# Performance work log

Hardware: AMD Instinct MI355X
Metric: run time of the kernel (lower is better)

The kernel has to match this reference:

```python
import jax, jax.numpy as jnp
import numpy as np

N_PIX = 4_194_304      # native emulator wavelength grid length
N_BINS = 350_000       # number of data wavelength bins (searchsorted labels)
MEDIAN_WL = 10500.0    # Angstroms, np.median(wl_bin_edges)
C_KMS = 299792.458     # speed of light, km/s
PI_SRC = 3.1415926654  # the (slightly off) pi literal used in the source
KERNEL_TAPS = 901      # torch.arange(-4.5, 4.51, 0.01)


def _conv_same(flux, kernel):
    """conv1d with padding='same'; kernels are symmetric so corr == conv."""
    half = kernel.shape[0] // 2
    out = jax.lax.conv_general_dilated(
        flux[None, None, :], kernel[None, None, :],
        window_strides=(1,), padding=[(half, half)])
    return out[0, 0]


def setup_inputs() -> dict:
    key = jax.random.key(0)
    k1, k2 = jax.random.split(key)
    return {
        "high_res_model": jax.random.uniform(k1, (N_PIX,), dtype=jnp.float32),
        "ln_sigma_angs": jnp.asarray(-2.3, dtype=jnp.float32),
        "ln_vsini": jnp.asarray(2.89, dtype=jnp.float32),
        "segment_ids": jnp.sort(jax.random.randint(k2, (N_PIX,), 0, N_BINS)),
    }


def reference(high_res_model, ln_sigma_angs, ln_vsini, segment_ids):
    dt = high_res_model.dtype
    grid = jnp.linspace(-4.5, 4.5, KERNEL_TAPS).astype(dt)
    sigma_angs = 0.01 + jnp.exp(ln_sigma_angs)
    vsini = 0.9 + jnp.exp(ln_vsini)

    # --- rotational broadening kernel ---
    x = (C_KMS * grid / MEDIAN_WL) / vsini
    x2 = jnp.minimum(x * x, 1.0)                     # torch.clamp(x2, max=1)
    inside = x2 < 0.99999999
    safe_x2 = jnp.where(inside, x2, 0.0)             # avoid sqrt(neg)/nan-grad
    rot_kernel = jnp.where(inside, 2.0 * jnp.sqrt(1.0 - safe_x2), 0.0)
    rot_kernel = rot_kernel / jnp.sum(rot_kernel)
    rot = _conv_same(high_res_model, rot_kernel)

    # --- instrumental (Gaussian) broadening kernel ---
    gauss = (1.0 / (sigma_angs * jnp.sqrt(jnp.asarray(2.0 * PI_SRC, dt)))
             * jnp.exp(-0.5 * grid * grid / (sigma_angs * sigma_angs)) * 0.01)
    conv = _conv_same(rot, gauss)

    # --- resample to data: fused segment mean (replaces split+per-bin mean) ---
    sums = jax.ops.segment_sum(conv, segment_ids, num_segments=N_BINS)
    counts = jax.ops.segment_sum(jnp.ones_like(conv), segment_ids,
                                 num_segments=N_BINS)
    means = sums / jnp.maximum(counts, 1.0)
    return jnp.clip(means, 0.0, 1.0)[1:-1]
```

## Files before the change

### kernel.cpp

```cpp
#include <hip/hip_runtime.h>
#include <hip/hip_bf16.h>

#define TAPS 901
#define CB 256
#define R 11
#define NGRP 22
#define NK (R * NGRP)
#define OPB (CB * R)
#define STAGE_N 3060
#define TILE 3072
#define WPAD 12

__device__ __forceinline__ float4 ld4(const float* p) {
  return *reinterpret_cast<const float4*>(p);
}

__global__ __launch_bounds__(1024) void prep(
    const float* __restrict__ lns, const float* __restrict__ lnv,
    const float* __restrict__ flux, const int* __restrict__ ids,
    float* __restrict__ comb_w, int* __restrict__ bounds,
    float* __restrict__ sums, int n) {
  __shared__ float rk[1024], gk[1024], red[1024];
  __shared__ float ck[2048];
  __shared__ int sb[8];
  const int t = threadIdx.x;
  if (t < 8) sb[t] = (t & 1) ? -1 : 4096;
  __syncthreads();

  const float sigma = 0.01f + expf(lns[0]);
  const float vsini = 0.9f + expf(lnv[0]);

  float rv = 0.f, gv = 0.f;
  if (t < TAPS) {
    float g = -4.5f + 0.01f * (float)t;
    float x = (299792.458f * g / 10500.0f) / vsini;
    float x2 = fminf(x * x, 1.0f);
    if (x2 < 1.0f) rv = 2.0f * sqrtf(1.0f - x2);
    gv = (1.0f / (sigma * sqrtf(2.0f * 3.1415926654f))) *
         expf(-0.5f * g * g / (sigma * sigma)) * 0.01f;
  }
  red[t] = rv;
  __syncthreads();
  for (int s = 512; s > 0; s >>= 1) {
    if (t < s) red[t] += red[t + s];
    __syncthreads();
  }
  const float rsum = red[0];

  const float rw = (t < TAPS) ? rv / rsum : 0.f;
  rk[t] = rw;
  gk[t] = gv;
  if (t < TAPS) {
    if (rw != 0.f)          { atomicMin(&sb[0], t); atomicMax(&sb[1], t); }
    if (fabsf(gv) > 1e-10f) { atomicMin(&sb[2], t); atomicMax(&sb[3], t); }
  }
  __syncthreads();
  const int rlo = sb[0], rhi = sb[1], glo = sb[2], ghi = sb[3];
  int flo = 450 - glo; if (flo < 0) flo = 0;
  int fhi = ghi - 450; if (fhi < 0) fhi = 0;

  if (blockIdx.x == 0) {
    for (int t2 = t; t2 < 2048; t2 += 1024) {
      float c = 0.f;
      if (t2 <= 1800) {
        int jmin = rlo > t2 - ghi ? rlo : t2 - ghi;
        int jmax = rhi < t2 - glo ? rhi : t2 - glo;
        for (int j = jmin; j <= jmax; ++j) c += rk[j] * gk[t2 - j];
      }
      ck[t2] = c;
      comb_w[t2] = c;
      if (t2 <= 1800 && fabsf(c) > 1e-12f) { atomicMin(&sb[4], t2); atomicMax(&sb[5], t2); }
    }
    __syncthreads();
    if (t == 0) {
      int clo = sb[4], chi = sb[5];
      if (chi < clo) { clo = 900; chi = 900; }
      while (chi - (clo & ~3) + 1 > NK) {
        if (fabsf(ck[clo]) <= fabsf(ck[chi])) ++clo; else --chi;
      }
      bounds[0] = clo & ~3; bounds[1] = flo; bounds[2] = fhi;
    }
  } else if (blockIdx.x == 1) {
    const int m = flo + fhi;
    float* rbuf = ck;
    for (int j = t; j < m; j += 1024) {
      float s = 0.f;
      int j0 = 450 - j > rlo ? 450 - j : rlo;
      for (int j2 = j0; j2 <= rhi; ++j2) s += rk[j2] * flux[j + j2 - 450];
      rbuf[j] = s;
    }
    __syncthreads();
    for (int i = t; i < flo; i += 1024) {
      float c = 0.f;
      int k0 = 450 - i > glo ? 450 - i : glo;
      for (int k = k0; k <= ghi; ++k) c += gk[k] * rbuf[i + k - 450];
      atomicAdd(&sums[ids[i]], c);
    }
  } else {
    const int m = flo + fhi;
    float* rbuf = ck;
    const int jbase = n - m;
    for (int jj = t; jj < m; jj += 1024) {
      int j = jbase + jj;
      float s = 0.f;
      int j2hi = n - 1 + 450 - j < rhi ? n - 1 + 450 - j : rhi;
      for (int j2 = rlo; j2 <= j2hi; ++j2) s += rk[j2] * flux[j + j2 - 450];
      rbuf[jj] = s;
    }
    __syncthreads();
    for (int ii = t; ii < fhi; ii += 1024) {
      int i = n - fhi + ii;
      float c = 0.f;
      int khi = n - 1 + 450 - i < ghi ? n - 1 + 450 - i : ghi;
      for (int k = glo; k <= khi; ++k) c += gk[k] * rbuf[i + k - 450 - jbase];
      atomicAdd(&sums[ids[i]], c);
    }
  }
}

__global__ __launch_bounds__(CB) void conv_scatter(
    const float* __restrict__ flux, const float* __restrict__ comb_w,
    const int* __restrict__ bounds, const int* __restrict__ ids,
    float* __restrict__ sums, int* __restrict__ bstart, int n, int nbins) {
  __shared__ __align__(16) float lds[TILE];
  __shared__ __align__(16) float wl[NGRP * WPAD];
  const int tid = threadIdx.x;
  const int clo4 = __builtin_amdgcn_readfirstlane(bounds[0]);
  const int flo  = __builtin_amdgcn_readfirstlane(bounds[1]);
  const int fhi  = __builtin_amdgcn_readfirstlane(bounds[2]);
  const int blockBase = blockIdx.x * OPB;
  const int start = blockBase - 900 + clo4;

  if (start >= 0 && start + STAGE_N <= n) {
    for (int j = tid * 4; j < STAGE_N; j += CB * 4)
      *reinterpret_cast<float4*>(&lds[j]) = ld4(flux + start + j);
  } else {
    for (int j = tid * 4; j < STAGE_N; j += CB * 4) {
      int g = start + j;
      float4 v;
      v.x = (unsigned)g       < (unsigned)n ? flux[g]     : 0.f;
      v.y = (unsigned)(g + 1) < (unsigned)n ? flux[g + 1] : 0.f;
      v.z = (unsigned)(g + 2) < (unsigned)n ? flux[g + 2] : 0.f;
      v.w = (unsigned)(g + 3) < (unsigned)n ? flux[g + 3] : 0.f;
      *reinterpret_cast<float4*>(&lds[j]) = v;
    }
  }
  for (int k = tid; k < NGRP * WPAD; k += CB) {
    const int g = k / WPAD, u = k % WPAD;
    wl[k] = (u < R) ? comb_w[clo4 + g * R + u] : 0.f;
  }
  __syncthreads();

  const int idx0 = tid * R;
  float win[R];
#pragma unroll
  for (int r = 0; r < R; ++r) win[r] = lds[idx0 + r];
  float acc[R];
#pragma unroll
  for (int r = 0; r < R; ++r) acc[r] = 0.f;

  const float4* wl4 = reinterpret_cast<const float4*>(wl);
#define TAP(u, wv)                                                     \
  {                                                                    \
    _Pragma("unroll") for (int r = 0; r < R; ++r)                      \
        acc[r] = fmaf(wv, win[((u) + r) % R], acc[r]);                 \
    win[u] = lds[idx0 + kk + (u) + R];                                 \
  }
  float4 n0 = wl4[0], n1 = wl4[1], n2 = wl4[2];
#pragma unroll 2
  for (int g = 0; g < NGRP; ++g) {
    const int kk = g * R;
    const float4 q0 = n0, q1 = n1, q2 = n2;
    if (g + 1 < NGRP) {
      n0 = wl4[(g + 1) * 3 + 0];
      n1 = wl4[(g + 1) * 3 + 1];
      n2 = wl4[(g + 1) * 3 + 2];
    }
    TAP(0, q0.x)  TAP(1, q0.y)  TAP(2, q0.z)  TAP(3, q0.w)
    TAP(4, q1.x)  TAP(5, q1.y)  TAP(6, q1.z)  TAP(7, q1.w)
    TAP(8, q2.x)  TAP(9, q2.y)  TAP(10, q2.z)
  }
#undef TAP

  const int base = blockBase + idx0;
  const int loskip = flo - base;
  const int hicap = (n - fhi) - base;
  int prev = (base > 0) ? ((base < n) ? ids[base - 1] : 0) : -1;
  int cur = -1; float run = 0.f;
#pragma unroll
  for (int r = 0; r < R; ++r) {
    const int p = base + r;
    if (p < n) {
      const int id = ids[p];
      if (id != prev) {
        for (int b = prev + 1; b <= id; ++b) bstart[b] = p;
        prev = id;
      }
      if (r >= loskip && r < hicap) {
        if (id == cur) {
          run += acc[r];
        } else {
          if (cur >= 0) atomicAdd(&sums[cur], run);
          cur = id; run = acc[r];
        }
      }
    }
  }
  if (cur >= 0) atomicAdd(&sums[cur], run);
  if (base < n && base + R > n - 1) {
    for (int b = prev + 1; b < nbins; ++b) bstart[b] = n;
  }
}

__global__ __launch_bounds__(256) void seg_mean(
    const float* __restrict__ sums, const int* __restrict__ bstart,
    float* __restrict__ out, int out_n) {
  const int gid = blockIdx.x * blockDim.x + threadIdx.x;
  if (gid >= out_n) return;
  const int b = gid + 1;
  const int c = bstart[b + 1] - bstart[b];
  const float mean = sums[b] / (float)(c > 1 ? c : 1);
  out[gid] = fminf(fmaxf(mean, 0.f), 1.f);
}

extern "C" void kernel_launch(void* const* d_in, const int* in_sizes, int n_in,
                              void* d_out, int out_size, void* d_ws,
                              size_t ws_size, hipStream_t stream) {
  const float* flux = (const float*)d_in[0];
  const float* lns  = (const float*)d_in[1];
  const float* lnv  = (const float*)d_in[2];
  const int*   ids  = (const int*)d_in[3];
  float* out = (float*)d_out;
  const int n = in_sizes[0];
  const int nbins = out_size + 2;

  float* ws      = (float*)d_ws;
  float* comb_w  = ws;
  int*   bounds  = (int*)(ws + 2048);
  float* sums    = ws + 2112;
  int*   bstart  = (int*)(sums + nbins);

  hipMemsetAsync(sums, 0, (size_t)nbins * sizeof(float), stream);
  prep<<<3, 1024, 0, stream>>>(lns, lnv, flux, ids, comb_w, bounds, sums, n);
  const int nblk = (n + OPB - 1) / OPB;
  conv_scatter<<<nblk, CB, 0, stream>>>(flux, comb_w, bounds, ids, sums,
                                        bstart, n, nbins);
  seg_mean<<<(out_size + 255) / 256, 256, 0, stream>>>(sums, bstart, out,
                                                       out_size);
}
```

Measured before the change: 138.6 us.

## Triple-buffer register windows and shrink outputs per thread to nine

The register-blocked convolution now gives each thread 9 outputs instead of 11, with 27 tap groups. The single rotating window is replaced by three register buffers that rotate across groups. The next buffer is loaded from LDS a whole group ahead, so LDS latency overlaps the FMAs and the modulo indexing disappears. A launch-bounds occupancy hint of 4 is added and the LDS tile shrinks, which trades more blocks and more redundant halo loading for lower register pressure.

Result: slower. 186.7 us (+34.7%).

```diff
diff --git a/kernel.cpp b/kernel.cpp
--- a/kernel.cpp
+++ b/kernel.cpp
@@ -3,12 +3,12 @@
 
 #define TAPS 901
 #define CB 256
-#define R 11
-#define NGRP 22
+#define R 9
+#define NGRP 27
 #define NK (R * NGRP)
 #define OPB (CB * R)
-#define STAGE_N 3060
-#define TILE 3072
+#define STAGE_E 2548
+#define TILE 2560
 #define WPAD 12
 
 __device__ __forceinline__ float4 ld4(const float* p) {
@@ -118,7 +118,7 @@
   }
 }
 
-__global__ __launch_bounds__(CB) void conv_scatter(
+__global__ __launch_bounds__(CB, 4) void conv_scatter(
     const float* __restrict__ flux, const float* __restrict__ comb_w,
     const int* __restrict__ bounds, const int* __restrict__ ids,
     float* __restrict__ sums, int* __restrict__ bstart, int n, int nbins) {
@@ -131,11 +131,11 @@
   const int blockBase = blockIdx.x * OPB;
   const int start = blockBase - 900 + clo4;
 
-  if (start >= 0 && start + STAGE_N <= n) {
-    for (int j = tid * 4; j < STAGE_N; j += CB * 4)
+  if (start >= 0 && start + STAGE_E <= n) {
+    for (int j = tid * 4; j < STAGE_E; j += CB * 4)
       *reinterpret_cast<float4*>(&lds[j]) = ld4(flux + start + j);
   } else {
-    for (int j = tid * 4; j < STAGE_N; j += CB * 4) {
+    for (int j = tid * 4; j < STAGE_E; j += CB * 4) {
       int g = start + j;
       float4 v;
       v.x = (unsigned)g       < (unsigned)n ? flux[g]     : 0.f;
@@ -152,35 +152,50 @@
   __syncthreads();
 
   const int idx0 = tid * R;
-  float win[R];
-#pragma unroll
-  for (int r = 0; r < R; ++r) win[r] = lds[idx0 + r];
+  float wA[R], wB[R], wC[R];
+#pragma unroll
+  for (int i = 0; i < R; ++i) wA[i] = lds[idx0 + i];
+#pragma unroll
+  for (int i = 0; i < R; ++i) wB[i] = lds[idx0 + R + i];
   float acc[R];
 #pragma unroll
   for (int r = 0; r < R; ++r) acc[r] = 0.f;
 
   const float4* wl4 = reinterpret_cast<const float4*>(wl);
-#define TAP(u, wv)                                                     \
-  {                                                                    \
-    _Pragma("unroll") for (int r = 0; r < R; ++r)                      \
-        acc[r] = fmaf(wv, win[((u) + r) % R], acc[r]);                 \
-    win[u] = lds[idx0 + kk + (u) + R];                                 \
-  }
-  float4 n0 = wl4[0], n1 = wl4[1], n2 = wl4[2];
-#pragma unroll 2
-  for (int g = 0; g < NGRP; ++g) {
-    const int kk = g * R;
-    const float4 q0 = n0, q1 = n1, q2 = n2;
-    if (g + 1 < NGRP) {
-      n0 = wl4[(g + 1) * 3 + 0];
-      n1 = wl4[(g + 1) * 3 + 1];
-      n2 = wl4[(g + 1) * 3 + 2];
-    }
-    TAP(0, q0.x)  TAP(1, q0.y)  TAP(2, q0.z)  TAP(3, q0.w)
-    TAP(4, q1.x)  TAP(5, q1.y)  TAP(6, q1.z)  TAP(7, q1.w)
-    TAP(8, q2.x)  TAP(9, q2.y)  TAP(10, q2.z)
-  }
-#undef TAP
+  float4 wn0 = wl4[0], wn1 = wl4[1];
+  float wn2 = wl[8];
+
+#define WSEL(u)                                                         \
+  ((u) < 4 ? ((u) == 0 ? q0.x : (u) == 1 ? q0.y : (u) == 2 ? q0.z : q0.w) \
+           : (u) < 8 ? ((u) == 4 ? q1.x : (u) == 5 ? q1.y : (u) == 6 ? q1.z : q1.w) \
+                     : q2)
+#define GRP(W0, W1, W2, GI)                                             \
+  {                                                                     \
+    const int kk = (GI) * R;                                            \
+    _Pragma("unroll") for (int i = 0; i < R; ++i)                       \
+        W2[i] = lds[idx0 + kk + 2 * R + i];    \
+    const float4 q0 = wn0, q1 = wn1;                                    \
+    const float q2 = wn2;                                               \
+    const int gn = ((GI) + 1 < NGRP) ? (GI) + 1 : 0;                    \
+    wn0 = wl4[gn * 3 + 0];                                              \
+    wn1 = wl4[gn * 3 + 1];                                              \
+    wn2 = wl[gn * WPAD + 8];                                            \
+    _Pragma("unroll") for (int u = 0; u < R; ++u) {                     \
+      const float wv = WSEL(u);                                         \
+      _Pragma("unroll") for (int r = 0; r < R; ++r) {                   \
+        const float val = (u + r < R) ? W0[u + r] : W1[u + r - R];      \
+        acc[r] = fmaf(wv, val, acc[r]);                                 \
+      }                                                                 \
+    }                                                                   \
+  }
+
+  for (int m = 0; m < NGRP / 3; ++m) {
+    GRP(wA, wB, wC, 3 * m)
+    GRP(wB, wC, wA, 3 * m + 1)
+    GRP(wC, wA, wB, 3 * m + 2)
+  }
+#undef GRP
+#undef WSEL
 
   const int base = blockBase + idx0;
   const int loskip = flo - base;
```
